# Kernel optimization log

Measured on AMD Instinct MI355X. Metric: run time of the kernel, lower is better.

The kernel has to match this reference:

```python
import jax, jax.numpy as jnp
import numpy as np
from jax import lax

N_VOX = 20000   # occupied voxels
T = 35          # cfg.VOXEL_POINT_COUNT
FIN = 7         # features_in
GX, GY, GZ = 128, 128, 10   # dense grid = cfg.X_SIZE/VOXEL_X_SIZE etc.
VFE1_OUT, VFE2_OUT = 32, 128
EPS = 1e-5


def _bn(x, g, b, axes):
    m = jnp.mean(x, axes, keepdims=True)
    v = jnp.var(x, axes, keepdims=True)
    return (x - m) * lax.rsqrt(v + EPS) * g + b


def _fcn(x2d, w, b, g, be):
    # Linear -> BatchNorm1d (batch stats) -> ReLU
    h = x2d @ w + b
    return jax.nn.relu(_bn(h, g, be, (0,)))


def _vfe(x, mask, w, b, g, be):
    n, t, _ = x.shape
    units = w.shape[1]
    pwf = _fcn(x.reshape(n * t, -1), w, b, g, be).reshape(n, t, units)
    laf = jnp.broadcast_to(jnp.max(pwf, axis=1, keepdims=True), pwf.shape)
    pwcf = jnp.concatenate([pwf, laf], axis=2)            # [n, t, 2*units]
    return pwcf * mask[:, :, None].astype(pwcf.dtype)


def _conv_bn_relu(x, w, b, g, be):
    y = lax.conv_general_dilated(x, w, (1, 1, 1), [(1, 1)] * 3,
                                 dimension_numbers=('NCDHW', 'OIDHW', 'NCDHW'))
    y = y + b[None, :, None, None, None]
    y = _bn(y, g[None, :, None, None, None], be[None, :, None, None, None], (0, 2, 3, 4))
    return jax.nn.relu(y)


def setup_inputs() -> dict:
    key = jax.random.key(0)
    ks = jax.random.split(key, 16)
    vf = jax.random.normal(ks[0], (N_VOX, T, FIN), dtype=jnp.float32)
    bidx = jnp.zeros((N_VOX,), jnp.int32)   # single frame: batch index 0
    cx = jax.random.randint(ks[1], (N_VOX,), 0, GX, dtype=jnp.int32)
    cy = jax.random.randint(ks[2], (N_VOX,), 0, GY, dtype=jnp.int32)
    cz = jax.random.randint(ks[3], (N_VOX,), 0, GZ, dtype=jnp.int32)
    coords = jnp.stack([bidx, cx, cy, cz], axis=1)

    def lin(k, cin, cout):
        return jax.random.normal(k, (cin, cout), jnp.float32) / np.float32(np.sqrt(cin))

    def conv(k, cout, cin):
        return jax.random.normal(k, (cout, cin, 3, 3, 3), jnp.float32) / np.float32(np.sqrt(cin * 27))

    p = {
        'vfe1_w': lin(ks[4], FIN, VFE1_OUT // 2), 'vfe1_b': jnp.zeros((VFE1_OUT // 2,)),
        'vfe1_g': jnp.ones((VFE1_OUT // 2,)), 'vfe1_be': jnp.zeros((VFE1_OUT // 2,)),
        'vfe2_w': lin(ks[5], VFE1_OUT, VFE2_OUT // 2), 'vfe2_b': jnp.zeros((VFE2_OUT // 2,)),
        'vfe2_g': jnp.ones((VFE2_OUT // 2,)), 'vfe2_be': jnp.zeros((VFE2_OUT // 2,)),
        'fcn_w': lin(ks[6], VFE2_OUT, VFE2_OUT), 'fcn_b': jnp.zeros((VFE2_OUT,)),
        'fcn_g': jnp.ones((VFE2_OUT,)), 'fcn_be': jnp.zeros((VFE2_OUT,)),
        'c1_w': conv(ks[7], 64, 128), 'c1_b': jnp.zeros((64,)), 'c1_g': jnp.ones((64,)), 'c1_be': jnp.zeros((64,)),
        'c2_w': conv(ks[8], 64, 64), 'c2_b': jnp.zeros((64,)), 'c2_g': jnp.ones((64,)), 'c2_be': jnp.zeros((64,)),
        'c3_w': conv(ks[9], 2, 64), 'c3_b': jnp.zeros((2,)), 'c3_g': jnp.ones((2,)), 'c3_be': jnp.zeros((2,)),
    }
    return {'voxel_features': vf, 'voxel_coords': coords, **p}


def reference(voxel_features, voxel_coords,
              vfe1_w, vfe1_b, vfe1_g, vfe1_be,
              vfe2_w, vfe2_b, vfe2_g, vfe2_be,
              fcn_w, fcn_b, fcn_g, fcn_be,
              c1_w, c1_b, c1_g, c1_be,
              c2_w, c2_b, c2_g, c2_be,
              c3_w, c3_b, c3_g, c3_be):
    mask = jnp.max(voxel_features, axis=2) != 0            # [N, T]
    x = _vfe(voxel_features, mask, vfe1_w, vfe1_b, vfe1_g, vfe1_be)   # [N, T, 32]
    x = _vfe(x, mask, vfe2_w, vfe2_b, vfe2_g, vfe2_be)                # [N, T, 128]
    n, t, _ = x.shape
    x = _fcn(x.reshape(n * t, -1), fcn_w, fcn_b, fcn_g, fcn_be).reshape(n, t, -1)
    x = jnp.max(x, axis=1)                                  # [N, 128] voxel-wise feature

    b, cx, cy, cz = voxel_coords[:, 0], voxel_coords[:, 1], voxel_coords[:, 2], voxel_coords[:, 3]
    dense = jnp.zeros((1, VFE2_OUT, GX, GY, GZ), x.dtype)
    dense = dense.at[b, :, cx, cy, cz].set(x)               # sparse -> dense scatter

    y = _conv_bn_relu(dense, c1_w, c1_b, c1_g, c1_be)
    y = _conv_bn_relu(y, c2_w, c2_b, c2_g, c2_be)
    y = _conv_bn_relu(y, c3_w, c3_b, c3_g, c3_be)           # [1, 2, GX, GY, GZ]

    sparse = y[b, :, cx, cy, cz]                            # dense -> sparse gather, [N, 2]
    return jax.nn.softmax(sparse, axis=1)
```

## Files before the change

kernel.cpp:

```cpp
#include <hip/hip_runtime.h>
#include <hip/hip_bf16.h>
#include <cstddef>
#include <cstdint>

#define TT 35
#define NVOX 20000
#define NTR 700000
#define FIN 7
#define GXD 128
#define GYD 128
#define GZD 10
#define NPOS 163840
#define BNEPS 1e-5f

#define S_BN1 0
#define S_BN2 64
#define S_BN3 320
#define S_C1  832
#define S_C2  1088
#define S_C3  1344
#define STATS_FLOATS 2048

#define O_STATS 0ull
#define O_ZERO  8192ull
#define O_OWNER 12288ull
#define O_H3MAX 667648ull
#define O_G     O_H3MAX
#define O_H3MIN 10907648ull
#define O_WB1   667648ull
#define O_WB2   1110016ull
#define O_DENSE 21147648ull
#define O_PC    O_DENSE
#define O_MKF   67284992ull
#define O_Y1    63090688ull
#define O_Y2    O_DENSE
#define O_Y3    O_H3MIN
#define WS_BYTES 84062208ull

typedef __attribute__((ext_vector_type(8))) short short8;
typedef __attribute__((ext_vector_type(4))) float f32x4;
typedef __attribute__((ext_vector_type(4))) int int4v;

__device__ __forceinline__ float bf2f(__hip_bfloat16 x) { return __bfloat162float(x); }
__device__ __forceinline__ __hip_bfloat16 f2bf(float x) { return __float2bfloat16(x); }
__device__ __forceinline__ float bfs2f(short s) {
    union { unsigned u; float f; } cv; cv.u = ((unsigned)(unsigned short)s) << 16; return cv.f;
}
__device__ __forceinline__ short f2bfs(float f) {
    __hip_bfloat16 h = __float2bfloat16(f);
    return *(short*)&h;
}

__global__ __launch_bounds__(256) void k_stats1(
    const float* __restrict__ vf, float* __restrict__ stats,
    const float* __restrict__ w1, const float* __restrict__ b1)
{
    __shared__ float w1s[112], b1s[16];
    __shared__ float ssum[16], ssq[16];
    int tid = threadIdx.x;
    for (int i = tid; i < 112; i += 256) w1s[i] = w1[i];
    if (tid < 16) { b1s[tid] = b1[tid]; ssum[tid] = 0.f; ssq[tid] = 0.f; }
    __syncthreads();

    float lsum[16], lsq[16];
#pragma unroll
    for (int u = 0; u < 16; ++u) { lsum[u] = 0.f; lsq[u] = 0.f; }

    for (int r = blockIdx.x * 256 + tid; r < NTR; r += gridDim.x * 256) {
        float v[FIN];
#pragma unroll
        for (int f = 0; f < FIN; ++f) v[f] = vf[(size_t)r * FIN + f];
#pragma unroll
        for (int u = 0; u < 16; ++u) {
            float h = b1s[u];
#pragma unroll
            for (int f = 0; f < FIN; ++f) h += v[f] * w1s[f * 16 + u];
            lsum[u] += h; lsq[u] += h * h;
        }
    }
#pragma unroll
    for (int u = 0; u < 16; ++u) {
        float a = lsum[u], b = lsq[u];
        for (int off = 32; off > 0; off >>= 1) {
            a += __shfl_down(a, off);
            b += __shfl_down(b, off);
        }
        if ((tid & 63) == 0) { atomicAdd(&ssum[u], a); atomicAdd(&ssq[u], b); }
    }
    __syncthreads();
    if (tid < 16) {
        atomicAdd(&stats[S_BN1 + tid], ssum[tid]);
        atomicAdd(&stats[S_BN1 + 16 + tid], ssq[tid]);
    }
}

__global__ void k_finalize(float* __restrict__ stats, int base, int C, float invM,
                           const float* __restrict__ g, const float* __restrict__ be)
{
    int i = threadIdx.x;
    if (i < C) {
        float mean = stats[base + i] * invM;
        float var  = stats[base + C + i] * invM - mean * mean;
        float sc = g[i] * rsqrtf(var + BNEPS);
        stats[base + 2 * C + i] = sc;
        stats[base + 3 * C + i] = be[i] - mean * sc;
    }
}

__device__ __forceinline__ void stage1(
    int tid, int n, const float* __restrict__ vf,
    const float* w1s, const float* b1s, const float* sc1, const float* sh1,
    float* pwf, float* laf, float* mk, float* pc)
{
    {
        int u = tid & 15, tg = tid >> 4;
        for (int t = tg; t < TT; t += 16) {
            const float* vr = vf + (size_t)(n * TT + t) * FIN;
            float vv[FIN];
#pragma unroll
            for (int f = 0; f < FIN; ++f) vv[f] = vr[f];
            float h = b1s[u];
#pragma unroll
            for (int f = 0; f < FIN; ++f) h += vv[f] * w1s[f * 16 + u];
            pwf[t * 16 + u] = fmaxf(h * sc1[u] + sh1[u], 0.f);
            if (u == 0) {
                float mx = vv[0];
#pragma unroll
                for (int f = 1; f < FIN; ++f) mx = fmaxf(mx, vv[f]);
                mk[t] = (mx != 0.f) ? 1.f : 0.f;
            }
        }
    }
    __syncthreads();
    if (tid < 16) {
        float m = pwf[tid];
        for (int t = 1; t < TT; ++t) m = fmaxf(m, pwf[t * 16 + tid]);
        laf[tid] = m;
    }
    __syncthreads();
    {
        int c = tid & 31, tg = tid >> 5;
        for (int t = tg; t < TT; t += 8)
            pc[t * 32 + c] = (c < 16 ? pwf[t * 16 + c] : laf[c - 16]) * mk[t];
    }
    __syncthreads();
}

__global__ __launch_bounds__(256) void k_pc(
    const float* __restrict__ vf, const float* __restrict__ stats,
    __hip_bfloat16* __restrict__ pcg, float* __restrict__ mkg,
    float* __restrict__ Gg,
    const float* __restrict__ w1, const float* __restrict__ b1)
{
    __shared__ float w1s[112], b1s[16], sc1[16], sh1[16];
    __shared__ float pwf[TT * 16], laf[16], mk[TT];
    __shared__ __align__(16) float pc[TT * 32];
    int tid = threadIdx.x;
    for (int i = tid; i < 112; i += 256) w1s[i] = w1[i];
    if (tid < 16) {
        b1s[tid] = b1[tid];
        sc1[tid] = stats[S_BN1 + 32 + tid];
        sh1[tid] = stats[S_BN1 + 48 + tid];
    }
    __syncthreads();

    int gi = tid >> 3, gj = (tid & 7) * 4;
    float ga0 = 0.f, ga1 = 0.f, ga2 = 0.f, ga3 = 0.f;
    float sacc = 0.f;

    for (int n = blockIdx.x; n < NVOX; n += gridDim.x) {
        stage1(tid, n, vf, w1s, b1s, sc1, sh1, pwf, laf, mk, pc);
        if (tid < 140) {
            int t = tid >> 2, part = tid & 3;
            short8 v;
#pragma unroll
            for (int j = 0; j < 8; ++j) v[j] = f2bfs(pc[t * 32 + part * 8 + j]);
            *(short8*)(pcg + ((size_t)n * TT + t) * 32 + part * 8) = v;
        }
        if (tid < TT) mkg[n * TT + tid] = mk[tid];
        for (int t = 0; t < TT; ++t) {
            float xi = pc[t * 32 + gi];
            f32x4 xj = *(const f32x4*)&pc[t * 32 + gj];
            ga0 += xi * xj[0]; ga1 += xi * xj[1];
            ga2 += xi * xj[2]; ga3 += xi * xj[3];
        }
        if (tid < 32) {
            float a = 0.f;
            for (int t = 0; t < TT; ++t) a += pc[t * 32 + tid];
            sacc += a;
        }
        __syncthreads();
    }
    atomicAdd(&Gg[gi * 32 + gj + 0], ga0);
    atomicAdd(&Gg[gi * 32 + gj + 1], ga1);
    atomicAdd(&Gg[gi * 32 + gj + 2], ga2);
    atomicAdd(&Gg[gi * 32 + gj + 3], ga3);
    if (tid < 32) atomicAdd(&Gg[1024 + tid], sacc);
}

__global__ void k_bn2g(const float* __restrict__ Gg,
                       const float* __restrict__ w2, const float* __restrict__ b2,
                       const float* __restrict__ g2, const float* __restrict__ be2,
                       float* __restrict__ stats)
{
    int u = threadIdx.x;
    if (u >= 64) return;
    float wc[32];
#pragma unroll
    for (int c = 0; c < 32; ++c) wc[c] = w2[c * 64 + u];
    float dot = 0.f;
#pragma unroll
    for (int c = 0; c < 32; ++c) dot += Gg[1024 + c] * wc[c];
    float quad = 0.f;
    for (int c = 0; c < 32; ++c) {
        float a = 0.f;
#pragma unroll
        for (int c2 = 0; c2 < 32; ++c2) a += Gg[c * 32 + c2] * wc[c2];
        quad += wc[c] * a;
    }
    float b = b2[u];
    float N = (float)NTR;
    float mean = (dot + N * b) / N;
    float q = quad + 2.f * b * dot + N * b * b;
    float var = q / N - mean * mean;
    float sc = g2[u] * rsqrtf(var + BNEPS);
    stats[S_BN2 + 128 + u] = sc;
    stats[S_BN2 + 192 + u] = be2[u] - mean * sc;
}

__global__ __launch_bounds__(256) void k_vfe3m(
    const __hip_bfloat16* __restrict__ pcg, const float* __restrict__ mkg,
    float* __restrict__ stats,
    float* __restrict__ h3max, float* __restrict__ h3min,
    const float* __restrict__ w2, const float* __restrict__ b2,
    const float* __restrict__ w3, const float* __restrict__ b3,
    const __hip_bfloat16* __restrict__ zp)
{
    __shared__ __align__(16) short pc2s[48 * 128];
    __shared__ float mkan[48];
    int tid = threadIdx.x;
    int l = tid & 63, w = tid >> 6;
    int lr = l & 15, lk = l >> 4;
    int cw2 = w * 16 + lr;

    short8 w2f;
#pragma unroll
    for (int j = 0; j < 8; ++j) w2f[j] = f2bfs(w2[(lk * 8 + j) * 64 + cw2]);
    int c3[2] = { (2 * w) * 16 + lr, (2 * w + 1) * 16 + lr };
    short8 w3f[2][4];
#pragma unroll
    for (int ni = 0; ni < 2; ++ni)
#pragma unroll
        for (int ks = 0; ks < 4; ++ks)
#pragma unroll
            for (int j = 0; j < 8; ++j)
                w3f[ni][ks][j] = f2bfs(w3[(ks * 32 + lk * 8 + j) * 128 + c3[ni]]);

    float sc2c = stats[S_BN2 + 128 + cw2], sh2c = stats[S_BN2 + 192 + cw2];
    float b2c = b2[cw2];
    float b3c[2] = { b3[c3[0]], b3[c3[1]] };
    float s3a[2] = { 0.f, 0.f }, q3a[2] = { 0.f, 0.f };

    if (tid < 48) mkan[tid] = 0.f;
    __syncthreads();

    char* pb = (char*)pc2s;
    for (int n = blockIdx.x; n < NVOX; n += gridDim.x) {
        if (tid < TT) mkan[tid] = mkg[n * TT + tid];
        f32x4 hacc[3];
#pragma unroll
        for (int mt = 0; mt < 3; ++mt) {
            int t = mt * 16 + lr;
            const short8* ap = (t < TT)
                ? (const short8*)(pcg + ((size_t)n * TT + t) * 32 + lk * 8)
                : (const short8*)zp;
            short8 a = *ap;
            hacc[mt] = { b2c, b2c, b2c, b2c };
            hacc[mt] = __builtin_amdgcn_mfma_f32_16x16x32_bf16(a, w2f, hacc[mt], 0, 0, 0);
        }
        float pw2[3][4];
#pragma unroll
        for (int mt = 0; mt < 3; ++mt)
#pragma unroll
            for (int r = 0; r < 4; ++r)
                pw2[mt][r] = fmaxf(hacc[mt][r] * sc2c + sh2c, 0.f);
        float lm = 0.f;
#pragma unroll
        for (int mt = 0; mt < 2; ++mt)
#pragma unroll
            for (int r = 0; r < 4; ++r) lm = fmaxf(lm, pw2[mt][r]);
        if (lk == 0) {
#pragma unroll
            for (int r = 0; r < 3; ++r) lm = fmaxf(lm, pw2[2][r]);
        }
        lm = fmaxf(lm, __shfl_xor(lm, 16));
        lm = fmaxf(lm, __shfl_xor(lm, 32));
        __syncthreads();
#pragma unroll
        for (int mt = 0; mt < 3; ++mt)
#pragma unroll
            for (int r = 0; r < 4; ++r) {
                int t = mt * 16 + lk * 4 + r;
                float mv = mkan[t];
                int swz = (t & 7) << 4;
                *(short*)(pb + t * 256 + ((2 * cw2) ^ swz)) = f2bfs(pw2[mt][r] * mv);
                *(short*)(pb + t * 256 + ((2 * (64 + cw2)) ^ swz)) = f2bfs(lm * mv);
            }
        __syncthreads();
        f32x4 acc3[2][3];
#pragma unroll
        for (int ni = 0; ni < 2; ++ni)
#pragma unroll
            for (int mt = 0; mt < 3; ++mt)
                acc3[ni][mt] = { b3c[ni], b3c[ni], b3c[ni], b3c[ni] };
#pragma unroll
        for (int mt = 0; mt < 3; ++mt) {
            int t = mt * 16 + lr;
            int swz = (t & 7) << 4;
            short8 a[4];
#pragma unroll
            for (int ks = 0; ks < 4; ++ks)
                a[ks] = *(const short8*)(pb + t * 256 + ((2 * (ks * 32 + lk * 8)) ^ swz));
#pragma unroll
            for (int ni = 0; ni < 2; ++ni)
#pragma unroll
                for (int ks = 0; ks < 4; ++ks)
                    acc3[ni][mt] = __builtin_amdgcn_mfma_f32_16x16x32_bf16(
                        a[ks], w3f[ni][ks], acc3[ni][mt], 0, 0, 0);
        }
#pragma unroll
        for (int ni = 0; ni < 2; ++ni) {
            float mx = -1e30f, mn = 1e30f, s = 0.f, q = 0.f;
#pragma unroll
            for (int mt = 0; mt < 3; ++mt)
#pragma unroll
                for (int r = 0; r < 4; ++r) {
                    int t = mt * 16 + lk * 4 + r;
                    if (t < TT) {
                        float h = acc3[ni][mt][r];
                        mx = fmaxf(mx, h); mn = fminf(mn, h);
                        s += h; q += h * h;
                    }
                }
            mx = fmaxf(mx, __shfl_xor(mx, 16)); mx = fmaxf(mx, __shfl_xor(mx, 32));
            mn = fminf(mn, __shfl_xor(mn, 16)); mn = fminf(mn, __shfl_xor(mn, 32));
            s += __shfl_xor(s, 16); s += __shfl_xor(s, 32);
            q += __shfl_xor(q, 16); q += __shfl_xor(q, 32);
            if (l < 16) {
                h3max[(size_t)n * 128 + c3[ni]] = mx;
                h3min[(size_t)n * 128 + c3[ni]] = mn;
                s3a[ni] += s; q3a[ni] += q;
            }
        }
    }
    if (l < 16) {
#pragma unroll
        for (int ni = 0; ni < 2; ++ni) {
            atomicAdd(&stats[S_BN3 + c3[ni]], s3a[ni]);
            atomicAdd(&stats[S_BN3 + 128 + c3[ni]], q3a[ni]);
        }
    }
}

__global__ void k_owner(const int* __restrict__ coords, int* __restrict__ owner)
{
    int n = blockIdx.x * 256 + threadIdx.x;
    if (n >= NVOX) return;
    int cx = coords[n * 4 + 1], cy = coords[n * 4 + 2], cz = coords[n * 4 + 3];
    atomicMax(&owner[(cx * GYD + cy) * GZD + cz], n);
}

__global__ __launch_bounds__(128) void k_scatter(
    const float* __restrict__ h3max, const float* __restrict__ h3min,
    const int* __restrict__ coords, const int* __restrict__ owner,
    const float* __restrict__ stats, __hip_bfloat16* __restrict__ dense)
{
    int n = blockIdx.x, k = threadIdx.x;
    int cx = coords[n * 4 + 1], cy = coords[n * 4 + 2], cz = coords[n * 4 + 3];
    int cell = (cx * GYD + cy) * GZD + cz;
    if (owner[cell] != n) return;
    float sc = stats[S_BN3 + 256 + k], sh = stats[S_BN3 + 384 + k];
    float h = (sc >= 0.f) ? h3max[(size_t)n * 128 + k] : h3min[(size_t)n * 128 + k];
    dense[(size_t)cell * 128 + k] = f2bf(fmaxf(h * sc + sh, 0.f));
}

__global__ void k_wcvt2(const float* __restrict__ src, __hip_bfloat16* __restrict__ dst,
                        int IC)
{
    int i = blockIdx.x * 256 + threadIdx.x;
    int total = 27 * 64 * IC;
    if (i >= total) return;
    int perd = 64 * IC;
    int d = i / perd, rem = i % perd;
    int kk = rem / 512;
    int rem2 = rem % 512;
    int oc = rem2 >> 3, j = rem2 & 7;
    int ch = (kk >> 2) * 32 + (kk & 3) * 8 + j;
    dst[i] = f2bf(src[((size_t)oc * IC + ch) * 27 + d]);
}

template <int IC>
__global__ __launch_bounds__(256) void k_convm(
    const __hip_bfloat16* __restrict__ in, const __hip_bfloat16* __restrict__ wbn,
    const float* __restrict__ bias, __hip_bfloat16* __restrict__ outp,
    float* __restrict__ sumAcc, float* __restrict__ sqAcc)
{
    constexpr int KS = IC / 32;
    constexpr int ROWB = IC * 2;
    constexpr int CPR = ROWB / 16;
    __shared__ __align__(16) char atile[69 * ROWB];
    __shared__ float ssum[64], ssq[64];
    int tid = threadIdx.x;
    if (tid < 64) { ssum[tid] = 0.f; ssq[tid] = 0.f; }
    if (tid < CPR) *(int4v*)(atile + 68 * ROWB + tid * 16) = int4v{0, 0, 0, 0};

    int l = tid & 63, wave = tid >> 6;
    int wm = wave >> 1, wn = wave & 1;
    int lr = l & 15, lk = l >> 4;

    int pbase = blockIdx.x * 64;
    int p0 = pbase + wm * 32 + lr;
    int p1 = p0 + 16;
    int z0 = p0 % 10, y0 = (p0 / 10) % 128, x0 = p0 / 1280;
    int z1 = p1 % 10, y1c = (p1 / 10) % 128, x1 = p1 / 1280;

    int oc0 = wn * 32 + lr, oc1 = oc0 + 16;
    const short8* wb8 = (const short8*)wbn;

    float bb0 = bias[oc0], bb1 = bias[oc1];
    f32x4 acc[2][2];
#pragma unroll
    for (int t = 0; t < 2; ++t) {
        acc[t][0] = { bb0, bb0, bb0, bb0 };
        acc[t][1] = { bb1, bb1, bb1, bb1 };
    }

    for (int g = 0; g < 9; ++g) {
        int dx = g / 3 - 1, dy = g % 3 - 1;
        int offg = (dx * 128 + dy) * 10;
        __syncthreads();
        for (int c = tid; c < 68 * CPR; c += 256) {
            int r = c / CPR, sub = c - r * CPR;
            int grow = pbase + offg - 1 + r;
            grow = grow < 0 ? 0 : (grow > NPOS - 1 ? NPOS - 1 : grow);
            int4v v = *(const int4v*)(in + (size_t)grow * IC + sub * 8);
            *(int4v*)(atile + r * ROWB + ((sub * 16) ^ ((r & 7) << 4))) = v;
        }
        __syncthreads();
        bool vxy0 = ((unsigned)(x0 + dx) < 128u) & ((unsigned)(y0 + dy) < 128u);
        bool vxy1 = ((unsigned)(x1 + dx) < 128u) & ((unsigned)(y1c + dy) < 128u);
#pragma unroll
        for (int dzi = 0; dzi < 3; ++dzi) {
            int dz = dzi - 1;
            int d = g * 3 + dzi;
            bool v0 = vxy0 & ((unsigned)(z0 + dz) < 10u);
            bool v1 = vxy1 & ((unsigned)(z1 + dz) < 10u);
            int ra0 = v0 ? (wm * 32 + lr + dz + 1) : 68;
            int ra1 = v1 ? (wm * 32 + 16 + lr + dz + 1) : 68;
            short8 a0[KS], a1[KS], b0[KS], b1[KS];
#pragma unroll
            for (int k = 0; k < KS; ++k) {
                size_t bi = ((size_t)(d * KS + k) * 4 + lk) * 64;
                b0[k] = wb8[bi + oc0];
                b1[k] = wb8[bi + oc1];
                int xb = lk * 16 + k * 64;
                a0[k] = *(const short8*)(atile + ra0 * ROWB + (xb ^ ((ra0 & 7) << 4)));
                a1[k] = *(const short8*)(atile + ra1 * ROWB + (xb ^ ((ra1 & 7) << 4)));
            }
#pragma unroll
            for (int k = 0; k < KS; ++k) {
                acc[0][0] = __builtin_amdgcn_mfma_f32_16x16x32_bf16(a0[k], b0[k], acc[0][0], 0, 0, 0);
                acc[0][1] = __builtin_amdgcn_mfma_f32_16x16x32_bf16(a0[k], b1[k], acc[0][1], 0, 0, 0);
                acc[1][0] = __builtin_amdgcn_mfma_f32_16x16x32_bf16(a1[k], b0[k], acc[1][0], 0, 0, 0);
                acc[1][1] = __builtin_amdgcn_mfma_f32_16x16x32_bf16(a1[k], b1[k], acc[1][1], 0, 0, 0);
            }
        }
    }

    float s0 = 0.f, q0 = 0.f, s1 = 0.f, q1 = 0.f;
#pragma unroll
    for (int t = 0; t < 2; ++t) {
#pragma unroll
        for (int r = 0; r < 4; ++r) {
            int prow = pbase + wm * 32 + t * 16 + lk * 4 + r;
            float v0c = acc[t][0][r], v1c = acc[t][1][r];
            outp[(size_t)prow * 64 + oc0] = f2bf(v0c);
            outp[(size_t)prow * 64 + oc1] = f2bf(v1c);
            s0 += v0c; q0 += v0c * v0c;
            s1 += v1c; q1 += v1c * v1c;
        }
    }
    s0 += __shfl_xor(s0, 16); s0 += __shfl_xor(s0, 32);
    q0 += __shfl_xor(q0, 16); q0 += __shfl_xor(q0, 32);
    s1 += __shfl_xor(s1, 16); s1 += __shfl_xor(s1, 32);
    q1 += __shfl_xor(q1, 16); q1 += __shfl_xor(q1, 32);
    if (l < 16) {
        atomicAdd(&ssum[oc0], s0); atomicAdd(&ssq[oc0], q0);
        atomicAdd(&ssum[oc1], s1); atomicAdd(&ssq[oc1], q1);
    }
    __syncthreads();
    if (tid < 64) {
        atomicAdd(&sumAcc[tid], ssum[tid]);
        atomicAdd(&sqAcc[tid], ssq[tid]);
    }
}

__global__ __launch_bounds__(256) void k_conv3(
    const __hip_bfloat16* __restrict__ in, const float* __restrict__ w,
    const float* __restrict__ bias, float* __restrict__ y3,
    float* __restrict__ sumAcc, float* __restrict__ sqAcc)
{
    __shared__ float wred[8];
    int tid = threadIdx.x;
    int p = blockIdx.x * 256 + tid;
    int z = p % 10, y = (p / 10) % 128, x = p / 1280;
    float a0 = bias[0], a1 = bias[1];
    for (int d = 0; d < 27; ++d) {
        int dx = d / 9 - 1, dy = (d / 3) % 3 - 1, dz = d % 3 - 1;
        if (!(((unsigned)(x + dx) < 128u) & ((unsigned)(y + dy) < 128u) & ((unsigned)(z + dz) < 10u)))
            continue;
        int off = (dx * 128 + dy) * 10 + dz;
        const short8* ip = (const short8*)(in + (size_t)(p + off) * 64);
#pragma unroll
        for (int cb = 0; cb < 8; ++cb) {
            short8 v = ip[cb];
#pragma unroll
            for (int j = 0; j < 8; ++j) {
                int ic = cb * 8 + j;
                float f = bfs2f(v[j]);
                a0 += f * w[(ic) * 27 + d];
                a1 += f * w[(64 + ic) * 27 + d];
            }
        }
    }
    y3[(size_t)p * 2 + 0] = a0;
    y3[(size_t)p * 2 + 1] = a1;

    float s0 = a0, q0 = a0 * a0, s1 = a1, q1 = a1 * a1;
    for (int o = 32; o > 0; o >>= 1) {
        s0 += __shfl_down(s0, o); q0 += __shfl_down(q0, o);
        s1 += __shfl_down(s1, o); q1 += __shfl_down(q1, o);
    }
    int wv = tid >> 6;
    if ((tid & 63) == 0) { wred[wv] = s0; wred[4 + wv] = q0; }
    __syncthreads();
    if ((tid & 63) == 0 && wv == 0) {
        atomicAdd(&sumAcc[0], wred[0] + wred[1] + wred[2] + wred[3]);
        atomicAdd(&sqAcc[0], wred[4] + wred[5] + wred[6] + wred[7]);
    }
    __syncthreads();
    if ((tid & 63) == 0) { wred[wv] = s1; wred[4 + wv] = q1; }
    __syncthreads();
    if ((tid & 63) == 0 && wv == 0) {
        atomicAdd(&sumAcc[1], wred[0] + wred[1] + wred[2] + wred[3]);
        atomicAdd(&sqAcc[1], wred[4] + wred[5] + wred[6] + wred[7]);
    }
}

__global__ void k_bnrelu_v(__hip_bfloat16* __restrict__ ybuf,
                           const float* __restrict__ stats, int base)
{
    const int C = 64;
    int nvec = NPOS * C / 8;
    short8* yv = (short8*)ybuf;
    for (int i = blockIdx.x * 256 + threadIdx.x; i < nvec; i += gridDim.x * 256) {
        int cb = (i & 7) * 8;
        short8 v = yv[i];
        short8 r;
#pragma unroll
        for (int j = 0; j < 8; ++j) {
            float f = bfs2f(v[j]) * stats[base + 2 * C + cb + j] + stats[base + 3 * C + cb + j];
            r[j] = f2bfs(fmaxf(f, 0.f));
        }
        yv[i] = r;
    }
}

__global__ void k_out(const float* __restrict__ y3, const int* __restrict__ coords,
                      const float* __restrict__ stats, float* __restrict__ out)
{
    int n = blockIdx.x * 256 + threadIdx.x;
    if (n >= NVOX) return;
    int cx = coords[n * 4 + 1], cy = coords[n * 4 + 2], cz = coords[n * 4 + 3];
    int cell = (cx * GYD + cy) * GZD + cz;
    float a = fmaxf(y3[(size_t)cell * 2 + 0] * stats[S_C3 + 4] + stats[S_C3 + 6], 0.f);
    float b = fmaxf(y3[(size_t)cell * 2 + 1] * stats[S_C3 + 5] + stats[S_C3 + 7], 0.f);
    float m = fmaxf(a, b);
    float e0 = expf(a - m), e1 = expf(b - m);
    float inv = 1.f / (e0 + e1);
    out[n * 2 + 0] = e0 * inv;
    out[n * 2 + 1] = e1 * inv;
}

extern "C" void kernel_launch(void* const* d_in, const int* in_sizes, int n_in,
                              void* d_out, int out_size, void* d_ws, size_t ws_size,
                              hipStream_t stream)
{
    const float* vf     = (const float*)d_in[0];
    const int*   coords = (const int*)d_in[1];
    const float* w1  = (const float*)d_in[2];
    const float* b1  = (const float*)d_in[3];
    const float* g1  = (const float*)d_in[4];
    const float* be1 = (const float*)d_in[5];
    const float* w2  = (const float*)d_in[6];
    const float* b2  = (const float*)d_in[7];
    const float* g2  = (const float*)d_in[8];
    const float* be2 = (const float*)d_in[9];
    const float* w3  = (const float*)d_in[10];
    const float* b3  = (const float*)d_in[11];
    const float* g3  = (const float*)d_in[12];
    const float* be3 = (const float*)d_in[13];
    const float* c1w = (const float*)d_in[14];
    const float* c1b = (const float*)d_in[15];
    const float* c1g = (const float*)d_in[16];
    const float* c1be= (const float*)d_in[17];
    const float* c2w = (const float*)d_in[18];
    const float* c2b = (const float*)d_in[19];
    const float* c2g = (const float*)d_in[20];
    const float* c2be= (const float*)d_in[21];
    const float* c3w = (const float*)d_in[22];
    const float* c3b = (const float*)d_in[23];
    const float* c3g = (const float*)d_in[24];
    const float* c3be= (const float*)d_in[25];

    if (ws_size < WS_BYTES) return;

    char* base = (char*)d_ws;
    float* stats = (float*)(base + O_STATS);
    __hip_bfloat16* zp = (__hip_bfloat16*)(base + O_ZERO);
    int*   owner = (int*)(base + O_OWNER);
    float* Gg    = (float*)(base + O_G);
    float* h3max = (float*)(base + O_H3MAX);
    float* h3min = (float*)(base + O_H3MIN);
    __hip_bfloat16* wb1 = (__hip_bfloat16*)(base + O_WB1);
    __hip_bfloat16* wb2 = (__hip_bfloat16*)(base + O_WB2);
    __hip_bfloat16* pcg = (__hip_bfloat16*)(base + O_PC);
    float* mkg          = (float*)(base + O_MKF);
    __hip_bfloat16* dense = (__hip_bfloat16*)(base + O_DENSE);
    __hip_bfloat16* y1    = (__hip_bfloat16*)(base + O_Y1);
    __hip_bfloat16* y2    = (__hip_bfloat16*)(base + O_Y2);
    float* y3             = (float*)(base + O_Y3);

    hipMemsetAsync(stats, 0, STATS_FLOATS * sizeof(float), stream);
    hipMemsetAsync((void*)zp, 0, 256, stream);
    hipMemsetAsync(owner, 0xFF, (size_t)NPOS * sizeof(int), stream);
    hipMemsetAsync(Gg, 0, 1056 * sizeof(float), stream);

    k_stats1<<<1024, 256, 0, stream>>>(vf, stats, w1, b1);
    k_finalize<<<1, 128, 0, stream>>>(stats, S_BN1, 16, 1.f / NTR, g1, be1);
    k_pc<<<2048, 256, 0, stream>>>(vf, stats, pcg, mkg, Gg, w1, b1);
    k_bn2g<<<1, 64, 0, stream>>>(Gg, w2, b2, g2, be2, stats);
    k_vfe3m<<<1024, 256, 0, stream>>>(pcg, mkg, stats, h3max, h3min,
                                      w2, b2, w3, b3, zp);
    k_finalize<<<1, 128, 0, stream>>>(stats, S_BN3, 128, 1.f / NTR, g3, be3);
    k_owner<<<(NVOX + 255) / 256, 256, 0, stream>>>(coords, owner);
    hipMemsetAsync((void*)dense, 0, (size_t)NPOS * 128 * sizeof(__hip_bfloat16), stream);
    k_scatter<<<NVOX, 128, 0, stream>>>(h3max, h3min, coords, owner, stats, dense);

    k_wcvt2<<<(64 * 128 * 27 + 255) / 256, 256, 0, stream>>>(c1w, wb1, 128);
    k_wcvt2<<<(64 * 64 * 27 + 255) / 256, 256, 0, stream>>>(c2w, wb2, 64);

    k_convm<128><<<NPOS / 64, 256, 0, stream>>>(dense, wb1, c1b, y1,
                                                &stats[S_C1], &stats[S_C1 + 64]);
    k_finalize<<<1, 128, 0, stream>>>(stats, S_C1, 64, 1.f / NPOS, c1g, c1be);
    k_bnrelu_v<<<1024, 256, 0, stream>>>(y1, stats, S_C1);

    k_convm<64><<<NPOS / 64, 256, 0, stream>>>(y1, wb2, c2b, y2,
                                               &stats[S_C2], &stats[S_C2 + 64]);
    k_finalize<<<1, 128, 0, stream>>>(stats, S_C2, 64, 1.f / NPOS, c2g, c2be);
    k_bnrelu_v<<<1024, 256, 0, stream>>>(y2, stats, S_C2);

    k_conv3<<<NPOS / 256, 256, 0, stream>>>(y2, c3w, c3b, y3,
                                            &stats[S_C3], &stats[S_C3 + 2]);
    k_finalize<<<1, 128, 0, stream>>>(stats, S_C3, 2, 1.f / NPOS, c3g, c3be);

    k_out<<<(NVOX + 255) / 256, 256, 0, stream>>>(y3, coords, stats, (float*)d_out);
}
```

Before: 864.1 us.

## Compute BN1 stats from input Gram matrix and batch voxels in VFE1 kernel

BN1 statistics now come from a 7x7 Gram matrix plus sums of the raw input, so the first pass no longer evaluates the 16-unit linear layer per point. The k_pc kernel processes 8 voxels per block with staged shared-memory loads instead of a grid-stride loop over single voxels. The 32x32 Gram for BN2 is assembled from block structure (pwf-pwf, pwf-laf, laf-laf terms) so less per-point work is needed. Computing variance as E[x^2]-mean^2 from Gram sums can lose precision in float.

```diff
diff --git a/kernel.cpp b/kernel.cpp
--- a/kernel.cpp
+++ b/kernel.cpp
@@ -12,6 +12,7 @@
 #define GZD 10
 #define NPOS 163840
 #define BNEPS 1e-5f
+#define VB 8
 
 #define S_BN1 0
 #define S_BN2 64
@@ -51,47 +52,77 @@
     return *(short*)&h;
 }
 
-__global__ __launch_bounds__(256) void k_stats1(
-    const float* __restrict__ vf, float* __restrict__ stats,
-    const float* __restrict__ w1, const float* __restrict__ b1)
-{
-    __shared__ float w1s[112], b1s[16];
-    __shared__ float ssum[16], ssq[16];
+__global__ __launch_bounds__(256) void k_gram7(
+    const float* __restrict__ vf, float* __restrict__ G7)
+{
+    __shared__ __align__(16) float vs[256 * 7];
+    __shared__ float ss[35];
     int tid = threadIdx.x;
-    for (int i = tid; i < 112; i += 256) w1s[i] = w1[i];
-    if (tid < 16) { b1s[tid] = b1[tid]; ssum[tid] = 0.f; ssq[tid] = 0.f; }
-    __syncthreads();
-
-    float lsum[16], lsq[16];
-#pragma unroll
-    for (int u = 0; u < 16; ++u) { lsum[u] = 0.f; lsq[u] = 0.f; }
-
-    for (int r = blockIdx.x * 256 + tid; r < NTR; r += gridDim.x * 256) {
-        float v[FIN];
-#pragma unroll
-        for (int f = 0; f < FIN; ++f) v[f] = vf[(size_t)r * FIN + f];
-#pragma unroll
-        for (int u = 0; u < 16; ++u) {
-            float h = b1s[u];
-#pragma unroll
-            for (int f = 0; f < FIN; ++f) h += v[f] * w1s[f * 16 + u];
-            lsum[u] += h; lsq[u] += h * h;
-        }
-    }
-#pragma unroll
-    for (int u = 0; u < 16; ++u) {
-        float a = lsum[u], b = lsq[u];
-        for (int off = 32; off > 0; off >>= 1) {
-            a += __shfl_down(a, off);
-            b += __shfl_down(b, off);
-        }
-        if ((tid & 63) == 0) { atomicAdd(&ssum[u], a); atomicAdd(&ssq[u], b); }
-    }
-    __syncthreads();
-    if (tid < 16) {
-        atomicAdd(&stats[S_BN1 + tid], ssum[tid]);
-        atomicAdd(&stats[S_BN1 + 16 + tid], ssq[tid]);
-    }
+    if (tid < 35) ss[tid] = 0.f;
+
+    float acc[35];
+#pragma unroll
+    for (int a = 0; a < 35; ++a) acc[a] = 0.f;
+
+    for (int base = blockIdx.x * 256; base < NTR; base += gridDim.x * 256) {
+        int nrows = NTR - base; if (nrows > 256) nrows = 256;
+        __syncthreads();
+        for (int i = tid; i < nrows * 7; i += 256) vs[i] = vf[(size_t)base * 7 + i];
+        __syncthreads();
+        if (tid < nrows) {
+            float v[7];
+#pragma unroll
+            for (int f = 0; f < 7; ++f) v[f] = vs[tid * 7 + f];
+            int k = 0;
+#pragma unroll
+            for (int i = 0; i < 7; ++i) {
+                acc[28 + i] += v[i];
+#pragma unroll
+                for (int j = i; j < 7; ++j) acc[k++] += v[i] * v[j];
+            }
+        }
+    }
+    __syncthreads();
+#pragma unroll
+    for (int a = 0; a < 35; ++a) {
+        float r = acc[a];
+        for (int o = 32; o > 0; o >>= 1) r += __shfl_down(r, o);
+        if ((tid & 63) == 0) atomicAdd(&ss[a], r);
+    }
+    __syncthreads();
+    if (tid < 35) atomicAdd(&G7[tid], ss[tid]);
+}
+
+__global__ void k_bn1g(const float* __restrict__ G7,
+                       const float* __restrict__ w1, const float* __restrict__ b1,
+                       const float* __restrict__ g1, const float* __restrict__ be1,
+                       float* __restrict__ stats)
+{
+    int u = threadIdx.x;
+    if (u >= 16) return;
+    float w[7];
+#pragma unroll
+    for (int f = 0; f < 7; ++f) w[f] = w1[f * 16 + u];
+    float dot = 0.f;
+#pragma unroll
+    for (int f = 0; f < 7; ++f) dot += G7[28 + f] * w[f];
+    float quad = 0.f;
+    int k = 0;
+#pragma unroll
+    for (int i = 0; i < 7; ++i)
+#pragma unroll
+        for (int j = i; j < 7; ++j) {
+            float gij = G7[k++];
+            quad += (i == j ? 1.f : 2.f) * w[i] * w[j] * gij;
+        }
+    float b = b1[u];
+    float N = (float)NTR;
+    float mean = (dot + N * b) / N;
+    float q = quad + 2.f * b * dot + N * b * b;
+    float var = q / N - mean * mean;
+    float sc = g1[u] * rsqrtf(var + BNEPS);
+    stats[S_BN1 + 32 + u] = sc;
+    stats[S_BN1 + 48 + u] = be1[u] - mean * sc;
 }
 
 __global__ void k_finalize(float* __restrict__ stats, int base, int C, float invM,
@@ -107,45 +138,6 @@
     }
 }
 
-__device__ __forceinline__ void stage1(
-    int tid, int n, const float* __restrict__ vf,
-    const float* w1s, const float* b1s, const float* sc1, const float* sh1,
-    float* pwf, float* laf, float* mk, float* pc)
-{
-    {
-        int u = tid & 15, tg = tid >> 4;
-        for (int t = tg; t < TT; t += 16) {
-            const float* vr = vf + (size_t)(n * TT + t) * FIN;
-            float vv[FIN];
-#pragma unroll
-            for (int f = 0; f < FIN; ++f) vv[f] = vr[f];
-            float h = b1s[u];
-#pragma unroll
-            for (int f = 0; f < FIN; ++f) h += vv[f] * w1s[f * 16 + u];
-            pwf[t * 16 + u] = fmaxf(h * sc1[u] + sh1[u], 0.f);
-            if (u == 0) {
-                float mx = vv[0];
-#pragma unroll
-                for (int f = 1; f < FIN; ++f) mx = fmaxf(mx, vv[f]);
-                mk[t] = (mx != 0.f) ? 1.f : 0.f;
-            }
-        }
-    }
-    __syncthreads();
-    if (tid < 16) {
-        float m = pwf[tid];
-        for (int t = 1; t < TT; ++t) m = fmaxf(m, pwf[t * 16 + tid]);
-        laf[tid] = m;
-    }
-    __syncthreads();
-    {
-        int c = tid & 31, tg = tid >> 5;
-        for (int t = tg; t < TT; t += 8)
-            pc[t * 32 + c] = (c < 16 ? pwf[t * 16 + c] : laf[c - 16]) * mk[t];
-    }
-    __syncthreads();
-}
-
 __global__ __launch_bounds__(256) void k_pc(
     const float* __restrict__ vf, const float* __restrict__ stats,
     __hip_bfloat16* __restrict__ pcg, float* __restrict__ mkg,
@@ -153,8 +145,10 @@
     const float* __restrict__ w1, const float* __restrict__ b1)
 {
     __shared__ float w1s[112], b1s[16], sc1[16], sh1[16];
-    __shared__ float pwf[TT * 16], laf[16], mk[TT];
-    __shared__ __align__(16) float pc[TT * 32];
+    __shared__ float vfs[VB * 35 * 7];
+    __shared__ float pwfs[VB * 35 * 17];
+    __shared__ float lafs[VB][16], s16[VB][16], cnt[VB];
+    __shared__ float mks[VB * 35];
     int tid = threadIdx.x;
     for (int i = tid; i < 112; i += 256) w1s[i] = w1[i];
     if (tid < 16) {
@@ -162,40 +156,91 @@
         sc1[tid] = stats[S_BN1 + 32 + tid];
         sh1[tid] = stats[S_BN1 + 48 + tid];
     }
-    __syncthreads();
-
-    int gi = tid >> 3, gj = (tid & 7) * 4;
-    float ga0 = 0.f, ga1 = 0.f, ga2 = 0.f, ga3 = 0.f;
-    float sacc = 0.f;
-
-    for (int n = blockIdx.x; n < NVOX; n += gridDim.x) {
-        stage1(tid, n, vf, w1s, b1s, sc1, sh1, pwf, laf, mk, pc);
-        if (tid < 140) {
-            int t = tid >> 2, part = tid & 3;
-            short8 v;
-#pragma unroll
-            for (int j = 0; j < 8; ++j) v[j] = f2bfs(pc[t * 32 + part * 8 + j]);
-            *(short8*)(pcg + ((size_t)n * TT + t) * 32 + part * 8) = v;
-        }
-        if (tid < TT) mkg[n * TT + tid] = mk[tid];
-        for (int t = 0; t < TT; ++t) {
-            float xi = pc[t * 32 + gi];
-            f32x4 xj = *(const f32x4*)&pc[t * 32 + gj];
-            ga0 += xi * xj[0]; ga1 += xi * xj[1];
-            ga2 += xi * xj[2]; ga3 += xi * xj[3];
-        }
-        if (tid < 32) {
-            float a = 0.f;
-            for (int t = 0; t < TT; ++t) a += pc[t * 32 + tid];
-            sacc += a;
-        }
-        __syncthreads();
-    }
-    atomicAdd(&Gg[gi * 32 + gj + 0], ga0);
-    atomicAdd(&Gg[gi * 32 + gj + 1], ga1);
-    atomicAdd(&Gg[gi * 32 + gj + 2], ga2);
-    atomicAdd(&Gg[gi * 32 + gj + 3], ga3);
-    if (tid < 32) atomicAdd(&Gg[1024 + tid], sacc);
+    int n0 = blockIdx.x * VB;
+
+    for (int i = tid; i < VB * 245; i += 256) vfs[i] = vf[(size_t)n0 * 245 + i];
+    __syncthreads();
+
+    for (int i = tid; i < VB * 560; i += 256) {
+        int v = i / 560, rem = i - v * 560;
+        int t = rem >> 4, u = rem & 15;
+        const float* vr = &vfs[(v * 35 + t) * 7];
+        float h = b1s[u];
+#pragma unroll
+        for (int f = 0; f < 7; ++f) h += vr[f] * w1s[f * 16 + u];
+        pwfs[(v * 35 + t) * 17 + u] = fmaxf(h * sc1[u] + sh1[u], 0.f);
+        if (u == 0) {
+            float mx = vr[0];
+#pragma unroll
+            for (int f = 1; f < 7; ++f) mx = fmaxf(mx, vr[f]);
+            mks[v * 35 + t] = (mx != 0.f) ? 1.f : 0.f;
+        }
+    }
+    __syncthreads();
+
+    if (tid < VB * 16) {
+        int v = tid >> 4, u = tid & 15;
+        float m = 0.f, s = 0.f, c = 0.f;
+        for (int t = 0; t < 35; ++t) {
+            float p = pwfs[(v * 35 + t) * 17 + u];
+            float mk = mks[v * 35 + t];
+            m = fmaxf(m, p);
+            s += p * mk;
+            if (u == 0) c += mk;
+        }
+        lafs[v][u] = m;
+        s16[v][u] = s;
+        if (u == 0) cnt[v] = c;
+    }
+    __syncthreads();
+
+    for (int c = tid; c < VB * 140; c += 256) {
+        int v = c / 140, rem = c - v * 140;
+        int t = rem >> 2, p = rem & 3;
+        float mk = mks[v * 35 + t];
+        short8 o;
+        if (p < 2) {
+#pragma unroll
+            for (int j = 0; j < 8; ++j)
+                o[j] = f2bfs(pwfs[(v * 35 + t) * 17 + p * 8 + j] * mk);
+        } else {
+#pragma unroll
+            for (int j = 0; j < 8; ++j)
+                o[j] = f2bfs(lafs[v][(p - 2) * 8 + j] * mk);
+        }
+        *(short8*)(pcg + ((size_t)(n0 + v) * 35 + t) * 32 + p * 8) = o;
+    }
+    for (int i = tid; i < VB * 35; i += 256) mkg[(size_t)n0 * 35 + i] = mks[i];
+
+    {
+        int i = tid >> 4, j = tid & 15;
+        float g = 0.f;
+        for (int r = 0; r < VB * 35; ++r)
+            g += mks[r] * pwfs[r * 17 + i] * pwfs[r * 17 + j];
+        atomicAdd(&Gg[i * 32 + j], g);
+
+        float tr = 0.f, br = 0.f;
+#pragma unroll
+        for (int v = 0; v < VB; ++v) {
+            tr += s16[v][i] * lafs[v][j];
+            br += cnt[v] * lafs[v][i] * lafs[v][j];
+        }
+        atomicAdd(&Gg[i * 32 + 16 + j], tr);
+        atomicAdd(&Gg[(16 + j) * 32 + i], tr);
+        atomicAdd(&Gg[(16 + i) * 32 + 16 + j], br);
+    }
+    if (tid < 16) {
+        float s = 0.f;
+#pragma unroll
+        for (int v = 0; v < VB; ++v) s += s16[v][tid];
+        atomicAdd(&Gg[1024 + tid], s);
+    } else if (tid < 32) {
+        int b = tid - 16;
+        float s = 0.f;
+#pragma unroll
+        for (int v = 0; v < VB; ++v) s += cnt[v] * lafs[v][b];
+        atomicAdd(&Gg[1024 + tid], s);
+    }
 }
 
 __global__ void k_bn2g(const float* __restrict__ Gg,
@@ -630,6 +675,7 @@
     __hip_bfloat16* zp = (__hip_bfloat16*)(base + O_ZERO);
     int*   owner = (int*)(base + O_OWNER);
     float* Gg    = (float*)(base + O_G);
+    float* G7    = Gg + 1088;
     float* h3max = (float*)(base + O_H3MAX);
     float* h3min = (float*)(base + O_H3MIN);
     __hip_bfloat16* wb1 = (__hip_bfloat16*)(base + O_WB1);
@@ -644,11 +690,11 @@
     hipMemsetAsync(stats, 0, STATS_FLOATS * sizeof(float), stream);
     hipMemsetAsync((void*)zp, 0, 256, stream);
     hipMemsetAsync(owner, 0xFF, (size_t)NPOS * sizeof(int), stream);
-    hipMemsetAsync(Gg, 0, 1056 * sizeof(float), stream);
-
-    k_stats1<<<1024, 256, 0, stream>>>(vf, stats, w1, b1);
-    k_finalize<<<1, 128, 0, stream>>>(stats, S_BN1, 16, 1.f / NTR, g1, be1);
-    k_pc<<<2048, 256, 0, stream>>>(vf, stats, pcg, mkg, Gg, w1, b1);
+    hipMemsetAsync(Gg, 0, 1152 * sizeof(float), stream);
+
+    k_gram7<<<1024, 256, 0, stream>>>(vf, G7);
+    k_bn1g<<<1, 64, 0, stream>>>(G7, w1, b1, g1, be1, stats);
+    k_pc<<<NVOX / VB, 256, 0, stream>>>(vf, stats, pcg, mkg, Gg, w1, b1);
     k_bn2g<<<1, 64, 0, stream>>>(Gg, w2, b2, g2, be2, stats);
     k_vfe3m<<<1024, 256, 0, stream>>>(pcg, mkg, stats, h3max, h3min,
                                       w2, b2, w3, b3, zp);
```

Result: faster. 804.3 us (-6.9%).
